# Performance work log

Hardware: AMD Instinct MI355X
Metric: run time of the kernel (lower is better)

Reference implementation:

```python
import jax, jax.numpy as jnp
import numpy as np

NEG_INF = -9e15  # mask value used by the original dense GAT
ALPHA = 0.2      # LeakyReLU negative slope


def _gat_layer(x, adj_mask, W, a1, a2, concat):
    # x: [N, F], W: [F, D], a1/a2: [D]
    Wh = x @ W                                   # [N, D]
    # e_ij = leakyrelu(a1.Wh_i + a2.Wh_j)
    e = jax.nn.leaky_relu((Wh @ a1)[:, None] + (Wh @ a2)[None, :], negative_slope=ALPHA)
    e = jnp.where(adj_mask, e, NEG_INF)          # [N, N]
    att = jax.nn.softmax(e, axis=1)              # masked row softmax
    h = att @ Wh                                 # [N, D]
    return jax.nn.elu(h) if concat else h


def setup_inputs() -> dict:
    key = jax.random.key(0)
    ks = jax.random.split(key, 8)
    N, F, D, H, O = 4096, 512, 64, 8, 128
    x = jax.random.normal(ks[0], (N, F), dtype=jnp.float32)
    adj = jax.random.randint(ks[1], (N, N), 0, 2, dtype=jnp.int32)
    # per-head params (stacked for vmap)
    W_heads = jax.random.normal(ks[2], (H, F, D), dtype=jnp.float32) * 0.05
    a1_heads = jax.random.normal(ks[3], (H, D), dtype=jnp.float32) * 0.05
    a2_heads = jax.random.normal(ks[4], (H, D), dtype=jnp.float32) * 0.05
    # output attention layer: in = H*D, out = O
    W_out = jax.random.normal(ks[5], (H * D, O), dtype=jnp.float32) * 0.05
    a1_out = jax.random.normal(ks[6], (O,), dtype=jnp.float32) * 0.05
    a2_out = jax.random.normal(ks[7], (O,), dtype=jnp.float32) * 0.05
    return {"x": x, "adj": adj, "W_heads": W_heads, "a1_heads": a1_heads,
            "a2_heads": a2_heads, "W_out": W_out, "a1_out": a1_out, "a2_out": a2_out}


def reference(x, adj, W_heads, a1_heads, a2_heads, W_out, a1_out, a2_out):
    adj_mask = adj > 0                           # [N, N] bool
    # multi-head attention (concat=True -> ELU), vmapped over heads
    heads = jax.vmap(lambda W, a1, a2: _gat_layer(x, adj_mask, W, a1, a2, True))(
        W_heads, a1_heads, a2_heads)             # [H, N, D]
    H, N, D = heads.shape
    h = jnp.transpose(heads, (1, 0, 2)).reshape(N, H * D)  # concat dim=1
    # dropout is identity at inference
    out = _gat_layer(h, adj_mask, W_out, a1_out, a2_out, False)  # [N, O]
    return out
```

## Files before the change

kernel.cpp:

```cpp
#include <hip/hip_runtime.h>
#include <hip/hip_bf16.h>
#include <cstdint>


using bf16_t = __bf16;
using bf16x4 = __attribute__((ext_vector_type(4))) __bf16;
using bf16x8 = __attribute__((ext_vector_type(8))) __bf16;
using f32x4  = __attribute__((ext_vector_type(4))) float;

#define LOG2E 1.44269504f
constexpr int NN = 4096;

__global__ __launch_bounds__(256) void pack_bits_k(const int* __restrict__ adj,
                                                   uint32_t* __restrict__ bitsT, int total) {
    int stride = gridDim.x * blockDim.x;
    for (int idx = blockIdx.x * blockDim.x + threadIdx.x; idx < total; idx += stride) {
        unsigned long long m = __ballot(adj[idx] > 0);
        int l = threadIdx.x & 63;
        int i = idx >> 12, j = idx & 4095;
        if (l == 0)        bitsT[(size_t)(j >> 5) * NN + i] = (uint32_t)m;
        else if (l == 32)  bitsT[(size_t)(j >> 5) * NN + i] = (uint32_t)(m >> 32);
    }
}

__global__ __launch_bounds__(256) void prep_k(const float* __restrict__ x,
                                              const float* __restrict__ Wh,
                                              const float* __restrict__ Wo,
                                              bf16_t* __restrict__ xb,
                                              bf16_t* __restrict__ WT1,
                                              bf16_t* __restrict__ WoutT) {
    const int NX = NN * 512, NW1 = 512 * 512, NW2 = 128 * 512;
    int stride = gridDim.x * blockDim.x;
    for (int t = blockIdx.x * blockDim.x + threadIdx.x; t < NX + NW1 + NW2; t += stride) {
        if (t < NX) {
            xb[t] = (bf16_t)x[t];
        } else if (t < NX + NW1) {
            int u = t - NX; int hd = u >> 9, f = u & 511; int h = hd >> 6, d = hd & 63;
            WT1[u] = (bf16_t)Wh[(h << 15) + (f << 6) + d];
        } else {
            int u = t - NX - NW1; int o = u >> 9, cc = u & 511;
            WoutT[u] = (bf16_t)Wo[cc * 128 + o];
        }
    }
}

template<int CS, int WC>
__global__ __launch_bounds__(256) void gemm_k(const bf16_t* __restrict__ A,
                                              const bf16_t* __restrict__ BT,
                                              bf16_t* __restrict__ VTt,
                                              float* __restrict__ Cp,
                                              const float* __restrict__ a1,
                                              const float* __restrict__ a2,
                                              float* __restrict__ g1,
                                              float* __restrict__ E2,
                                              float* __restrict__ F2,
                                              int K, int NC, int kslice, int NCOLS) {
    const int wave = threadIdx.x >> 6, lane = threadIdx.x & 63;
    const int lr = lane & 15, kg = lane >> 4;
    const int rowb = (blockIdx.x * 4 + wave) * 16, cb = blockIdx.y * 64, kz = blockIdx.z;
    f32x4 acc[4];
#pragma unroll
    for (int dt = 0; dt < 4; ++dt) acc[dt] = 0.0f;
    const bf16_t* Ap = A + (size_t)(rowb + lr) * K;
    const int k0beg = kz * kslice, k0end = k0beg + kslice;
    for (int k0 = k0beg; k0 < k0end; k0 += 32) {
        bf16x8 af = *(const bf16x8*)(Ap + k0 + kg * 8);
#pragma unroll
        for (int dt = 0; dt < 4; ++dt) {
            bf16x8 bfr = *(const bf16x8*)(BT + (size_t)(cb + dt * 16 + lr) * K + k0 + kg * 8);
            acc[dt] = __builtin_amdgcn_mfma_f32_16x16x32_bf16(af, bfr, acc[dt], 0, 0, 0);
        }
    }
    if (WC) {
#pragma unroll
        for (int dt = 0; dt < 4; ++dt)
#pragma unroll
            for (int r = 0; r < 4; ++r)
                Cp[((size_t)kz * NN + rowb + kg * 4 + r) * NC + cb + dt * 16 + lr] = acc[dt][r];
    }
    if (CS) {
        const int i0 = rowb + kg * 4;
        const size_t tbase = (size_t)(i0 >> 5) * NCOLS * 32 + (i0 & 31);
#pragma unroll
        for (int dt = 0; dt < 4; ++dt) {
            bf16x4 v;
#pragma unroll
            for (int r = 0; r < 4; ++r) v[r] = (bf16_t)acc[dt][r];
            *(bf16x4*)(VTt + tbase + (size_t)(cb + dt * 16 + lr) * 32) = v;
        }
        float a1v[4], a2v[4];
#pragma unroll
        for (int dt = 0; dt < 4; ++dt) {
            a1v[dt] = a1[cb + dt * 16 + lr];
            a2v[dt] = a2[cb + dt * 16 + lr];
        }
#pragma unroll
        for (int r = 0; r < 4; ++r) {
            float d1 = 0.f, d2 = 0.f;
#pragma unroll
            for (int dt = 0; dt < 4; ++dt) { d1 += acc[dt][r] * a1v[dt]; d2 += acc[dt][r] * a2v[dt]; }
#pragma unroll
            for (int o = 1; o < 16; o <<= 1) { d1 += __shfl_xor(d1, o); d2 += __shfl_xor(d2, o); }
            if (lr == 0) {
                size_t row = (size_t)blockIdx.y * NN + rowb + kg * 4 + r;
                g1[row] = exp2f(-0.8f * LOG2E * d1);
                E2[row] = exp2f(LOG2E * d2);
                F2[row] = exp2f(0.2f * LOG2E * d2);
            }
        }
    }
}

template<int JZG>
__global__ __launch_bounds__(256) void gat_agg_k(const float* __restrict__ g1,
                                                 const float* __restrict__ E2,
                                                 const float* __restrict__ F2, int shead,
                                                 const uint32_t* __restrict__ bitsT,
                                                 const bf16_t* __restrict__ VTt,
                                                 bf16_t* __restrict__ Hpart,
                                                 float* __restrict__ zpart,
                                                 int CT, int JR, int ZC, int TS) {
    const int wave = threadIdx.x >> 6, lane = threadIdx.x & 63;
    const int lr = lane & 15, kg = lane >> 4;
    const int c = blockIdx.x / JZG, jzg = blockIdx.x % JZG;
    const int rowb = blockIdx.y * 64;
    const int jz = jzg * 4 + wave;
    const int cb = c * 64;
    const float* gp  = g1 + (size_t)shead * c;
    const float* E2p = E2 + (size_t)shead * c;
    const float* F2p = F2 + (size_t)shead * c;
    const int steps = JR >> 5, jb0 = jz * JR;

    f32x4 acc[4][4], accz[4];
#pragma unroll
    for (int rt = 0; rt < 4; ++rt) {
        accz[rt] = 0.0f;
#pragma unroll
        for (int dt = 0; dt < 4; ++dt) acc[rt][dt] = 0.0f;
    }
    float gv[4];
#pragma unroll
    for (int rt = 0; rt < 4; ++rt) gv[rt] = gp[rowb + rt * 16 + lr];
    bf16x8 ones;
#pragma unroll
    for (int e = 0; e < 8; ++e) ones[e] = (bf16_t)(lr == 0 ? 1.0f : 0.0f);

    auto LOAD = [&](int jb, bf16x8* bfr, f32x4& e2a, f32x4& e2b, f32x4& f2a, f32x4& f2b,
                    uint32_t* bw) {
        const int jk = jb + kg * 8;
        const int jc = jb >> 5;
        e2a = *(const f32x4*)(E2p + jk);
        e2b = *(const f32x4*)(E2p + jk + 4);
        f2a = *(const f32x4*)(F2p + jk);
        f2b = *(const f32x4*)(F2p + jk + 4);
        const bf16_t* vb = VTt + (size_t)jc * TS + kg * 8;
#pragma unroll
        for (int dt = 0; dt < 4; ++dt)
            bfr[dt] = *(const bf16x8*)(vb + (size_t)(cb + dt * 16 + lr) * 32);
        const uint32_t* bb = bitsT + (size_t)jc * NN + rowb;
#pragma unroll
        for (int rt = 0; rt < 4; ++rt)
            bw[rt] = bb[rt * 16 + lr];
    };
    auto COMP = [&](const bf16x8* bfr, f32x4 e2a, f32x4 e2b, f32x4 f2a, f32x4 f2b,
                    const uint32_t* bw) {
#pragma unroll
        for (int rt = 0; rt < 4; ++rt) {
            uint32_t mb = (bw[rt] >> (kg * 8)) & 0xffu;
            bf16x8 af;
#pragma unroll
            for (int e = 0; e < 8; ++e) {
                float e2 = (e < 4) ? e2a[e] : e2b[e - 4];
                float f2 = (e < 4) ? f2a[e] : f2b[e - 4];
                float p = fmaxf(e2, gv[rt] * f2);
                p = (mb & (1u << e)) ? p : 0.0f;
                af[e] = (bf16_t)p;
            }
#pragma unroll
            for (int dt = 0; dt < 4; ++dt)
                acc[rt][dt] = __builtin_amdgcn_mfma_f32_16x16x32_bf16(af, bfr[dt], acc[rt][dt], 0, 0, 0);
            accz[rt] = __builtin_amdgcn_mfma_f32_16x16x32_bf16(af, ones, accz[rt], 0, 0, 0);
        }
    };

    bf16x8 bA[4], bB[4];
    f32x4 eaA, ebA, faA, fbA, eaB, ebB, faB, fbB;
    uint32_t wA[4], wB[4];
    LOAD(jb0, bA, eaA, ebA, faA, fbA, wA);
    for (int js = 0; js < steps - 2; js += 2) {
        LOAD(jb0 + (js + 1) * 32, bB, eaB, ebB, faB, fbB, wB);
        COMP(bA, eaA, ebA, faA, fbA, wA);
        LOAD(jb0 + (js + 2) * 32, bA, eaA, ebA, faA, fbA, wA);
        COMP(bB, eaB, ebB, faB, fbB, wB);
    }
    LOAD(jb0 + (steps - 1) * 32, bB, eaB, ebB, faB, fbB, wB);
    COMP(bA, eaA, ebA, faA, fbA, wA);
    COMP(bB, eaB, ebB, faB, fbB, wB);

    bf16_t* Hp = Hpart + (size_t)jz * NN * CT;
#pragma unroll
    for (int rt = 0; rt < 4; ++rt) {
#pragma unroll
        for (int dt = 0; dt < 4; ++dt)
#pragma unroll
            for (int r = 0; r < 4; ++r)
                Hp[(size_t)(rowb + rt * 16 + kg * 4 + r) * CT + cb + dt * 16 + lr] = (bf16_t)acc[rt][dt][r];
    }
    if (lr == 0 && (ZC > 1 || c == 0)) {
        int zi = jz * ZC + (ZC > 1 ? c : 0);
#pragma unroll
        for (int rt = 0; rt < 4; ++rt)
#pragma unroll
            for (int r = 0; r < 4; ++r)
                zpart[(size_t)zi * NN + rowb + rt * 16 + kg * 4 + r] = accz[rt][r];
    }
}

__global__ __launch_bounds__(256) void fin1_k(const bf16_t* __restrict__ Hpart,
                                              const float* __restrict__ zpart,
                                              bf16_t* __restrict__ hcatb) {
    int idx = blockIdx.x * 256 + threadIdx.x;
    int i = idx >> 6, col0 = (idx & 63) << 3, h = col0 >> 6;
    float Z = 0.f;
#pragma unroll
    for (int jz = 0; jz < 8; ++jz) Z += zpart[(size_t)(jz * 8 + h) * NN + i];
    float hs[8];
#pragma unroll
    for (int e = 0; e < 8; ++e) hs[e] = 0.f;
#pragma unroll
    for (int jz = 0; jz < 8; ++jz) {
        bf16x8 v = *(const bf16x8*)(Hpart + ((size_t)jz * NN + i) * 512 + col0);
#pragma unroll
        for (int e = 0; e < 8; ++e) hs[e] += (float)v[e];
    }
    float invZ = 1.0f / Z;
    bf16x8 o;
#pragma unroll
    for (int e = 0; e < 8; ++e) {
        float v = hs[e] * invZ;
        o[e] = (bf16_t)(v > 0.f ? v : expm1f(v));
    }
    *(bf16x8*)(hcatb + (size_t)i * 512 + col0) = o;
}

__global__ __launch_bounds__(128) void comb2_k(const float* __restrict__ Cp,
                                               const float* __restrict__ a1o,
                                               const float* __restrict__ a2o,
                                               bf16_t* __restrict__ VT2t,
                                               float* __restrict__ g1o,
                                               float* __restrict__ E2o,
                                               float* __restrict__ F2o) {
    int r = blockIdx.x, t = threadIdx.x;
    float w = 0.f;
#pragma unroll
    for (int z = 0; z < 4; ++z) w += Cp[((size_t)z * NN + r) * 128 + t];
    VT2t[(size_t)(r >> 5) * (128 * 32) + t * 32 + (r & 31)] = (bf16_t)w;
    float d1 = w * a1o[t], d2 = w * a2o[t];
#pragma unroll
    for (int o = 1; o < 64; o <<= 1) { d1 += __shfl_xor(d1, o); d2 += __shfl_xor(d2, o); }
    __shared__ float red[4];
    if ((t & 63) == 0) { red[(t >> 6) * 2 + 0] = d1; red[(t >> 6) * 2 + 1] = d2; }
    __syncthreads();
    if (t == 0) {
        float s1 = red[0] + red[2], s2 = red[1] + red[3];
        g1o[r] = exp2f(-0.8f * LOG2E * s1);
        E2o[r] = exp2f(LOG2E * s2);
        F2o[r] = exp2f(0.2f * LOG2E * s2);
    }
}

__global__ __launch_bounds__(256) void fin2_k(const bf16_t* __restrict__ Hpart,
                                              const float* __restrict__ zpart,
                                              float* __restrict__ out) {
    int idx = blockIdx.x * 256 + threadIdx.x;
    int i = idx >> 4, col0 = (idx & 15) << 3;
    float Z = 0.f;
#pragma unroll
    for (int jz = 0; jz < 16; ++jz) Z += zpart[(size_t)jz * NN + i];
    float hs[8];
#pragma unroll
    for (int e = 0; e < 8; ++e) hs[e] = 0.f;
#pragma unroll
    for (int jz = 0; jz < 16; ++jz) {
        bf16x8 v = *(const bf16x8*)(Hpart + ((size_t)jz * NN + i) * 128 + col0);
#pragma unroll
        for (int e = 0; e < 8; ++e) hs[e] += (float)v[e];
    }
    float invZ = 1.0f / Z;
    f32x4 o0, o1;
#pragma unroll
    for (int e = 0; e < 4; ++e) { o0[e] = hs[e] * invZ; o1[e] = hs[e + 4] * invZ; }
    *(f32x4*)(out + (size_t)i * 128 + col0) = o0;
    *(f32x4*)(out + (size_t)i * 128 + col0 + 4) = o1;
}

extern "C" void kernel_launch(void* const* d_in, const int* in_sizes, int n_in,
                              void* d_out, int out_size, void* d_ws, size_t ws_size,
                              hipStream_t stream) {
    const int N = 4096;
    const float* x       = (const float*)d_in[0];
    const int*   adj     = (const int*)d_in[1];
    const float* W_heads = (const float*)d_in[2];
    const float* a1h     = (const float*)d_in[3];
    const float* a2h     = (const float*)d_in[4];
    const float* W_out   = (const float*)d_in[5];
    const float* a1o     = (const float*)d_in[6];
    const float* a2o     = (const float*)d_in[7];
    (void)in_sizes; (void)n_in; (void)out_size; (void)ws_size;

    size_t off = 0;
    auto alloc = [&](size_t bytes) { size_t o = off; off = (off + bytes + 255) & ~(size_t)255; return o; };
    char* ws = (char*)d_ws;
    uint32_t* bitsT = (uint32_t*)(ws + alloc((size_t)N * N / 8));
    bf16_t* VT1t    = (bf16_t*)(ws + alloc((size_t)512 * N * 2));
    bf16_t* hcatb   = (bf16_t*)(ws + alloc((size_t)N * 512 * 2));
    bf16_t* WoutT   = (bf16_t*)(ws + alloc((size_t)128 * 512 * 2));
    float*  g1h     = (float*)(ws + alloc((size_t)8 * N * 4));
    float*  E2h     = (float*)(ws + alloc((size_t)8 * N * 4));
    float*  F2h     = (float*)(ws + alloc((size_t)8 * N * 4));
    float*  g1o     = (float*)(ws + alloc((size_t)N * 4));
    float*  E2o     = (float*)(ws + alloc((size_t)N * 4));
    float*  F2o     = (float*)(ws + alloc((size_t)N * 4));
    bf16_t* VT2t    = (bf16_t*)(ws + alloc((size_t)128 * N * 2));
    float*  zpart   = (float*)(ws + alloc((size_t)64 * N * 4));
    bf16_t* Hpart   = (bf16_t*)(ws + alloc((size_t)32 * 1024 * 1024));
    bf16_t* xb    = (bf16_t*)Hpart;
    bf16_t* WT1   = (bf16_t*)((char*)Hpart + (4 << 20));
    float*  Cpart = (float*)Hpart;

    hipLaunchKernelGGL(pack_bits_k, dim3(2048), dim3(256), 0, stream, adj, bitsT, N * N);
    hipLaunchKernelGGL(prep_k, dim3(1024), dim3(256), 0, stream, x, W_heads, W_out, xb, WT1, WoutT);
    hipLaunchKernelGGL((gemm_k<1, 0>), dim3(64, 8, 1), dim3(256), 0, stream,
                       xb, WT1, VT1t, (float*)nullptr, a1h, a2h, g1h, E2h, F2h, 512, 512, 512, 512);
    hipLaunchKernelGGL((gat_agg_k<2>), dim3(16, 64, 1), dim3(256), 0, stream,
                       g1h, E2h, F2h, N, bitsT, VT1t, Hpart, zpart, 512, 512, 8, 512 * 32);
    hipLaunchKernelGGL(fin1_k, dim3(1024), dim3(256), 0, stream, Hpart, zpart, hcatb);
    hipLaunchKernelGGL((gemm_k<0, 1>), dim3(64, 2, 4), dim3(256), 0, stream,
                       hcatb, WoutT, (bf16_t*)nullptr, Cpart,
                       (const float*)nullptr, (const float*)nullptr,
                       (float*)nullptr, (float*)nullptr, (float*)nullptr, 512, 128, 128, 128);
    hipLaunchKernelGGL(comb2_k, dim3(4096), dim3(128), 0, stream, Cpart, a1o, a2o, VT2t, g1o, E2o, F2o);
    hipLaunchKernelGGL((gat_agg_k<4>), dim3(8, 64, 1), dim3(256), 0, stream,
                       g1o, E2o, F2o, 0, bitsT, VT2t, Hpart, zpart, 128, 256, 1, 128 * 32);
    hipLaunchKernelGGL(fin2_k, dim3(256), dim3(256), 0, stream, Hpart, zpart, (float*)d_out);
}
```

Measured before the change: 141.0 us.

## Replace packed adjacency bitmask with byte mask and AND-based masking

Instead of packing the adjacency into a transposed 1-bit-per-edge array, the preprocessing kernel now writes a byte-per-edge mask (0xFF or 0) in column-chunk-major layout. The aggregation kernel loads 8 mask bytes per row and uses byte-permute expansion to AND the bf16 attention values directly. This removes the per-element bit test and select. In exchange the mask grows eightfold to 16 MB, so both aggregation passes read much more mask traffic. The xb/WT1 scratch offset is moved so the workspace regions still fit.

```diff
diff --git a/kernel.cpp b/kernel.cpp
--- a/kernel.cpp
+++ b/kernel.cpp
@@ -7,19 +7,44 @@
 using bf16x4 = __attribute__((ext_vector_type(4))) __bf16;
 using bf16x8 = __attribute__((ext_vector_type(8))) __bf16;
 using f32x4  = __attribute__((ext_vector_type(4))) float;
+using u32x4  = __attribute__((ext_vector_type(4))) uint32_t;
 
 #define LOG2E 1.44269504f
 constexpr int NN = 4096;
 
-__global__ __launch_bounds__(256) void pack_bits_k(const int* __restrict__ adj,
-                                                   uint32_t* __restrict__ bitsT, int total) {
+__device__ inline uint32_t expand01(uint32_t b) {
+#if __has_builtin(__builtin_amdgcn_perm)
+    return __builtin_amdgcn_perm(0u, b, 0x01010000u);
+#else
+    return ((b & 0xFFu) * 0x101u) | ((((b >> 8) & 0xFFu) * 0x101u) << 16);
+#endif
+}
+__device__ inline uint32_t expand23(uint32_t b) {
+#if __has_builtin(__builtin_amdgcn_perm)
+    return __builtin_amdgcn_perm(0u, b, 0x03030202u);
+#else
+    return (((b >> 16) & 0xFFu) * 0x101u) | ((((b >> 24) & 0xFFu) * 0x101u) << 16);
+#endif
+}
+
+__global__ __launch_bounds__(256) void expand_k(const int* __restrict__ adj,
+                                                uint8_t* __restrict__ mask8) {
+    const int total8 = NN * NN / 8;
     int stride = gridDim.x * blockDim.x;
-    for (int idx = blockIdx.x * blockDim.x + threadIdx.x; idx < total; idx += stride) {
-        unsigned long long m = __ballot(adj[idx] > 0);
-        int l = threadIdx.x & 63;
-        int i = idx >> 12, j = idx & 4095;
-        if (l == 0)        bitsT[(size_t)(j >> 5) * NN + i] = (uint32_t)m;
-        else if (l == 32)  bitsT[(size_t)(j >> 5) * NN + i] = (uint32_t)(m >> 32);
+    for (int t = blockIdx.x * blockDim.x + threadIdx.x; t < total8; t += stride) {
+        size_t d = (size_t)t * 8;
+        int jc = (int)(d >> 17);
+        int rem = (int)(d & 131071);
+        int i = rem >> 5, j0 = rem & 31;
+        const int* ap = adj + (size_t)i * NN + jc * 32 + j0;
+        int4 a0 = *(const int4*)ap;
+        int4 a1 = *(const int4*)(ap + 4);
+        uint32_t w0 = (a0.x > 0 ? 0xFFu : 0u) | ((a0.y > 0 ? 0xFFu : 0u) << 8) |
+                      ((a0.z > 0 ? 0xFFu : 0u) << 16) | ((a0.w > 0 ? 0xFFu : 0u) << 24);
+        uint32_t w1 = (a1.x > 0 ? 0xFFu : 0u) | ((a1.y > 0 ? 0xFFu : 0u) << 8) |
+                      ((a1.z > 0 ? 0xFFu : 0u) << 16) | ((a1.w > 0 ? 0xFFu : 0u) << 24);
+        uint2 w; w.x = w0; w.y = w1;
+        *(uint2*)(mask8 + d) = w;
     }
 }
 
@@ -115,7 +140,7 @@
 __global__ __launch_bounds__(256) void gat_agg_k(const float* __restrict__ g1,
                                                  const float* __restrict__ E2,
                                                  const float* __restrict__ F2, int shead,
-                                                 const uint32_t* __restrict__ bitsT,
+                                                 const uint8_t* __restrict__ mask8,
                                                  const bf16_t* __restrict__ VTt,
                                                  bf16_t* __restrict__ Hpart,
                                                  float* __restrict__ zpart,
@@ -146,7 +171,7 @@
     for (int e = 0; e < 8; ++e) ones[e] = (bf16_t)(lr == 0 ? 1.0f : 0.0f);
 
     auto LOAD = [&](int jb, bf16x8* bfr, f32x4& e2a, f32x4& e2b, f32x4& f2a, f32x4& f2b,
-                    uint32_t* bw) {
+                    uint2* mk) {
         const int jk = jb + kg * 8;
         const int jc = jb >> 5;
         e2a = *(const f32x4*)(E2p + jk);
@@ -157,25 +182,29 @@
 #pragma unroll
         for (int dt = 0; dt < 4; ++dt)
             bfr[dt] = *(const bf16x8*)(vb + (size_t)(cb + dt * 16 + lr) * 32);
-        const uint32_t* bb = bitsT + (size_t)jc * NN + rowb;
+        const uint8_t* mp = mask8 + (size_t)jc * (NN * 32) + (size_t)(rowb + lr) * 32 + kg * 8;
 #pragma unroll
         for (int rt = 0; rt < 4; ++rt)
-            bw[rt] = bb[rt * 16 + lr];
+            mk[rt] = *(const uint2*)(mp + rt * 512);
     };
     auto COMP = [&](const bf16x8* bfr, f32x4 e2a, f32x4 e2b, f32x4 f2a, f32x4 f2b,
-                    const uint32_t* bw) {
+                    const uint2* mk) {
 #pragma unroll
         for (int rt = 0; rt < 4; ++rt) {
-            uint32_t mb = (bw[rt] >> (kg * 8)) & 0xffu;
-            bf16x8 af;
+            bf16x8 raw;
 #pragma unroll
             for (int e = 0; e < 8; ++e) {
                 float e2 = (e < 4) ? e2a[e] : e2b[e - 4];
                 float f2 = (e < 4) ? f2a[e] : f2b[e - 4];
-                float p = fmaxf(e2, gv[rt] * f2);
-                p = (mb & (1u << e)) ? p : 0.0f;
-                af[e] = (bf16_t)p;
+                raw[e] = (bf16_t)fmaxf(e2, gv[rt] * f2);
             }
+            u32x4 ru = __builtin_bit_cast(u32x4, raw);
+#pragma unroll
+            for (int p = 0; p < 4; ++p) {
+                uint32_t mb = (p < 2) ? mk[rt].x : mk[rt].y;
+                ru[p] &= (p & 1) ? expand23(mb) : expand01(mb);
+            }
+            bf16x8 af = __builtin_bit_cast(bf16x8, ru);
 #pragma unroll
             for (int dt = 0; dt < 4; ++dt)
                 acc[rt][dt] = __builtin_amdgcn_mfma_f32_16x16x32_bf16(af, bfr[dt], acc[rt][dt], 0, 0, 0);
@@ -185,17 +214,17 @@
 
     bf16x8 bA[4], bB[4];
     f32x4 eaA, ebA, faA, fbA, eaB, ebB, faB, fbB;
-    uint32_t wA[4], wB[4];
-    LOAD(jb0, bA, eaA, ebA, faA, fbA, wA);
+    uint2 mA[4], mB[4];
+    LOAD(jb0, bA, eaA, ebA, faA, fbA, mA);
     for (int js = 0; js < steps - 2; js += 2) {
-        LOAD(jb0 + (js + 1) * 32, bB, eaB, ebB, faB, fbB, wB);
-        COMP(bA, eaA, ebA, faA, fbA, wA);
-        LOAD(jb0 + (js + 2) * 32, bA, eaA, ebA, faA, fbA, wA);
-        COMP(bB, eaB, ebB, faB, fbB, wB);
-    }
-    LOAD(jb0 + (steps - 1) * 32, bB, eaB, ebB, faB, fbB, wB);
-    COMP(bA, eaA, ebA, faA, fbA, wA);
-    COMP(bB, eaB, ebB, faB, fbB, wB);
+        LOAD(jb0 + (js + 1) * 32, bB, eaB, ebB, faB, fbB, mB);
+        COMP(bA, eaA, ebA, faA, fbA, mA);
+        LOAD(jb0 + (js + 2) * 32, bA, eaA, ebA, faA, fbA, mA);
+        COMP(bB, eaB, ebB, faB, fbB, mB);
+    }
+    LOAD(jb0 + (steps - 1) * 32, bB, eaB, ebB, faB, fbB, mB);
+    COMP(bA, eaA, ebA, faA, fbA, mA);
+    COMP(bB, eaB, ebB, faB, fbB, mB);
 
     bf16_t* Hp = Hpart + (size_t)jz * NN * CT;
 #pragma unroll
@@ -311,7 +340,7 @@
     size_t off = 0;
     auto alloc = [&](size_t bytes) { size_t o = off; off = (off + bytes + 255) & ~(size_t)255; return o; };
     char* ws = (char*)d_ws;
-    uint32_t* bitsT = (uint32_t*)(ws + alloc((size_t)N * N / 8));
+    uint8_t* mask8  = (uint8_t*)(ws + alloc((size_t)N * N));
     bf16_t* VT1t    = (bf16_t*)(ws + alloc((size_t)512 * N * 2));
     bf16_t* hcatb   = (bf16_t*)(ws + alloc((size_t)N * 512 * 2));
     bf16_t* WoutT   = (bf16_t*)(ws + alloc((size_t)128 * 512 * 2));
@@ -325,15 +354,15 @@
     float*  zpart   = (float*)(ws + alloc((size_t)64 * N * 4));
     bf16_t* Hpart   = (bf16_t*)(ws + alloc((size_t)32 * 1024 * 1024));
     bf16_t* xb    = (bf16_t*)Hpart;
-    bf16_t* WT1   = (bf16_t*)((char*)Hpart + (4 << 20));
+    bf16_t* WT1   = (bf16_t*)((char*)Hpart + (9 << 20));
     float*  Cpart = (float*)Hpart;
 
-    hipLaunchKernelGGL(pack_bits_k, dim3(2048), dim3(256), 0, stream, adj, bitsT, N * N);
+    hipLaunchKernelGGL(expand_k, dim3(2048), dim3(256), 0, stream, adj, mask8);
     hipLaunchKernelGGL(prep_k, dim3(1024), dim3(256), 0, stream, x, W_heads, W_out, xb, WT1, WoutT);
     hipLaunchKernelGGL((gemm_k<1, 0>), dim3(64, 8, 1), dim3(256), 0, stream,
                        xb, WT1, VT1t, (float*)nullptr, a1h, a2h, g1h, E2h, F2h, 512, 512, 512, 512);
     hipLaunchKernelGGL((gat_agg_k<2>), dim3(16, 64, 1), dim3(256), 0, stream,
-                       g1h, E2h, F2h, N, bitsT, VT1t, Hpart, zpart, 512, 512, 8, 512 * 32);
+                       g1h, E2h, F2h, N, mask8, VT1t, Hpart, zpart, 512, 512, 8, 512 * 32);
     hipLaunchKernelGGL(fin1_k, dim3(1024), dim3(256), 0, stream, Hpart, zpart, hcatb);
     hipLaunchKernelGGL((gemm_k<0, 1>), dim3(64, 2, 4), dim3(256), 0, stream,
                        hcatb, WoutT, (bf16_t*)nullptr, Cpart,
@@ -341,6 +370,6 @@
                        (float*)nullptr, (float*)nullptr, (float*)nullptr, 512, 128, 128, 128);
     hipLaunchKernelGGL(comb2_k, dim3(4096), dim3(128), 0, stream, Cpart, a1o, a2o, VT2t, g1o, E2o, F2o);
     hipLaunchKernelGGL((gat_agg_k<4>), dim3(8, 64, 1), dim3(256), 0, stream,
-                       g1o, E2o, F2o, 0, bitsT, VT2t, Hpart, zpart, 128, 256, 1, 128 * 32);
+                       g1o, E2o, F2o, 0, mask8, VT2t, Hpart, zpart, 128, 256, 1, 128 * 32);
     hipLaunchKernelGGL(fin2_k, dim3(256), dim3(256), 0, stream, Hpart, zpart, (float*)d_out);
 }
```

After: 151.7 us. +7.6%, slower.
